# Performance work log

Hardware: AMD Instinct MI355X
Metric: run time of the kernel (lower is better)

## Reference

```python
import jax, jax.numpy as jnp
import numpy as np
import math

E = 2048         # n_embd
H = 16           # num query head pairs (num_heads)
HKV = 8          # num_kv_heads
NREP = H // HKV  # 2
HD = E // H // 2 # head_dim = 64
DEPTH = 12
LAMBDA_INIT = 0.8 - 0.6 * math.exp(-0.3 * DEPTH)
EPS = 1e-6


def setup_inputs() -> dict:
    key = jax.random.key(0)
    ks = jax.random.split(key, 10)
    s = lambda fan_in: 1.0 / np.sqrt(fan_in)
    return {
        "x": jax.random.normal(ks[0], (2, 2048, E), jnp.float32),
        "Wq": jax.random.normal(ks[1], (E, E), jnp.float32) * s(E),
        "Wk": jax.random.normal(ks[2], (E, E // NREP), jnp.float32) * s(E),
        "Wv": jax.random.normal(ks[3], (E, E // NREP), jnp.float32) * s(E),
        "Wo": jax.random.normal(ks[4], (E, E), jnp.float32) * s(E),
        "lam_q1": jax.random.normal(ks[5], (HD,), jnp.float32) * 0.1,
        "lam_k1": jax.random.normal(ks[6], (HD,), jnp.float32) * 0.1,
        "lam_q2": jax.random.normal(ks[7], (HD,), jnp.float32) * 0.1,
        "lam_k2": jax.random.normal(ks[8], (HD,), jnp.float32) * 0.1,
        "g": jnp.ones((2 * HD,), jnp.float32),  # RMSNorm weight
    }


def _rotary(x, cos, sin):
    # x: [B, T, nh, HD]; cos/sin: [T, HD//2]
    d = x.shape[-1] // 2
    x1, x2 = x[..., :d], x[..., d:]
    c = cos[None, :, None, :]
    si = sin[None, :, None, :]
    return jnp.concatenate([x1 * c + x2 * si, -x1 * si + x2 * c], axis=-1)


def reference(x, Wq, Wk, Wv, Wo, lam_q1, lam_k1, lam_q2, lam_k2, g):
    B, T, _ = x.shape
    q = (x @ Wq).reshape(B, T, 2 * H, HD)
    k = (x @ Wk).reshape(B, T, 2 * HKV, HD)
    v = (x @ Wv).reshape(B, T, HKV, 2 * HD)

    inv_freq = 1.0 / (10000.0 ** (jnp.arange(0, HD, 2, dtype=jnp.float32) / HD))
    freqs = jnp.arange(T, dtype=jnp.float32)[:, None] * inv_freq[None, :]
    cos, sin = jnp.cos(freqs), jnp.sin(freqs)
    q = _rotary(q, cos, sin)
    k = _rotary(k, cos, sin)

    q = jnp.transpose(q, (0, 2, 1, 3)) * (HD ** -0.5)   # [B, 2H, T, HD]
    k = jnp.repeat(jnp.transpose(k, (0, 2, 1, 3)), NREP, axis=1)  # [B, 2H, T, HD]
    v = jnp.repeat(jnp.transpose(v, (0, 2, 1, 3)), NREP, axis=1)  # [B, H, T, 2HD]

    scores = jnp.einsum('bhtd,bhsd->bhts', q, k)
    scores = jnp.nan_to_num(scores)
    mask = jnp.triu(jnp.full((T, T), -jnp.inf, scores.dtype), 1)
    scores = scores + mask
    p = jax.nn.softmax(scores.astype(jnp.float32), axis=-1).astype(scores.dtype)

    lam1 = jnp.exp(jnp.sum(lam_q1 * lam_k1))
    lam2 = jnp.exp(jnp.sum(lam_q2 * lam_k2))
    lam = lam1 - lam2 + LAMBDA_INIT

    p = p.reshape(B, H, 2, T, T)
    diff = p[:, :, 0] - lam * p[:, :, 1]               # [B, H, T, T]
    attn = jnp.einsum('bhts,bhsd->bhtd', diff, v)      # [B, H, T, 2HD]

    # RMSNorm over last dim (2*HD)
    attn = attn * jax.lax.rsqrt(jnp.mean(attn * attn, axis=-1, keepdims=True) + EPS) * g
    attn = attn * (1.0 - LAMBDA_INIT)
    attn = jnp.transpose(attn, (0, 2, 1, 3)).reshape(B, T, E)
    return attn @ Wo
```

## Files before the change

### kernel.cpp

```cpp
#include <hip/hip_runtime.h>

#define T_SEQ 2048

typedef __bf16 bf16x8 __attribute__((ext_vector_type(8)));
typedef float f32x4 __attribute__((ext_vector_type(4)));
typedef unsigned short u16;

__device__ __forceinline__ u16 f2b(float f) {
  unsigned u = __float_as_uint(f);
  unsigned r = 0x7fffu + ((u >> 16) & 1u);
  return (u16)((u + r) >> 16);
}
__device__ __forceinline__ float b2f(u16 v) {
  return __uint_as_float(((unsigned)v) << 16);
}
__device__ __forceinline__ f32x4 mfma16(bf16x8 a, bf16x8 b, f32x4 c) {
  return __builtin_amdgcn_mfma_f32_16x16x32_bf16(a, b, c, 0, 0, 0);
}
__device__ __forceinline__ void glds16(const void* g, void* s) {
  __builtin_amdgcn_global_load_lds(
      (const __attribute__((address_space(1))) void*)(uintptr_t)g,
      (__attribute__((address_space(3))) void*)(unsigned)(uintptr_t)s, 16, 0, 0);
}

__global__ void lam_kernel(const float* __restrict__ q1, const float* __restrict__ k1,
                           const float* __restrict__ q2, const float* __restrict__ k2,
                           float* __restrict__ outp) {
  int l = threadIdx.x;
  float a = q1[l] * k1[l];
  float c = q2[l] * k2[l];
  #pragma unroll
  for (int off = 32; off > 0; off >>= 1) {
    a += __shfl_down(a, off);
    c += __shfl_down(c, off);
  }
  if (l == 0) outp[0] = expf(a) - expf(c) + 0.7836057665316244f;
}

__global__ __launch_bounds__(256) void convert_kernel(const float* __restrict__ in,
                                                      u16* __restrict__ outp, int n) {
  int i = (blockIdx.x * 256 + threadIdx.x) * 4;
  if (i >= n) return;
  float4 v = *(const float4*)(in + i);
  ushort4 pk;
  pk.x = f2b(v.x); pk.y = f2b(v.y); pk.z = f2b(v.z); pk.w = f2b(v.w);
  *(ushort4*)(outp + i) = pk;
}

__global__ __launch_bounds__(256) void transpose_kernel(const float* __restrict__ in,
                                                        u16* __restrict__ outp, int R, int C) {
  __shared__ float tile[32][33];
  int c0 = blockIdx.x * 32, r0 = blockIdx.y * 32;
  int tx = threadIdx.x & 31, ty = threadIdx.x >> 5;
  #pragma unroll
  for (int k2 = 0; k2 < 4; k2++)
    tile[ty * 4 + k2][tx] = in[(size_t)(r0 + ty * 4 + k2) * C + c0 + tx];
  __syncthreads();
  #pragma unroll
  for (int k2 = 0; k2 < 4; k2++)
    outp[(size_t)(c0 + ty * 4 + k2) * R + r0 + tx] = f2b(tile[tx][ty * 4 + k2]);
}

template <bool OUT_BF16>
__global__ __launch_bounds__(256) void gemm128_kernel(const u16* __restrict__ A,
                                                      const u16* __restrict__ BT,
                                                      void* __restrict__ C, int N, int K) {
  __shared__ alignas(16) u16 As[128 * 64];
  __shared__ alignas(16) u16 Bs[128 * 64];
  const int tid = threadIdx.x, w = tid >> 6, lane = tid & 63;
  const int l15 = lane & 15, quad = lane >> 4;
  const int m0 = blockIdx.y * 128, n0 = blockIdx.x * 128;
  const int wm = (w >> 1) * 64, wn = (w & 1) * 64;
  const int lr = lane >> 3, slot = lane & 7, csw = slot ^ lr;
  f32x4 acc[4][4];
  #pragma unroll
  for (int mt = 0; mt < 4; mt++)
    #pragma unroll
    for (int nt = 0; nt < 4; nt++) acc[mt][nt] = (f32x4){0.f, 0.f, 0.f, 0.f};
  const u16* Ag = A + (size_t)(m0 + w * 32 + lr) * K + csw * 8;
  const u16* Bg = BT + (size_t)(n0 + w * 32 + lr) * K + csw * 8;
  u16* Asd = As + (w * 32) * 64;
  u16* Bsd = Bs + (w * 32) * 64;
  for (int kt = 0; kt < K; kt += 64) {
    #pragma unroll
    for (int i = 0; i < 4; i++) {
      glds16(Ag + kt + (size_t)(i * 8) * K, Asd + i * 512);
      glds16(Bg + kt + (size_t)(i * 8) * K, Bsd + i * 512);
    }
    __syncthreads();
    #pragma unroll
    for (int kk = 0; kk < 2; kk++) {
      bf16x8 am[4], bn[4];
      #pragma unroll
      for (int t = 0; t < 4; t++) {
        const int ra = wm + t * 16 + l15;
        am[t] = *(const bf16x8*)&As[ra * 64 + (((kk * 4 + quad) ^ (ra & 7)) << 3)];
        const int rb = wn + t * 16 + l15;
        bn[t] = *(const bf16x8*)&Bs[rb * 64 + (((kk * 4 + quad) ^ (rb & 7)) << 3)];
      }
      #pragma unroll
      for (int mt = 0; mt < 4; mt++)
        #pragma unroll
        for (int nt = 0; nt < 4; nt++) acc[mt][nt] = mfma16(am[mt], bn[nt], acc[mt][nt]);
    }
    __syncthreads();
  }
  const int row = m0 + wm + quad * 4;
  #pragma unroll
  for (int mt = 0; mt < 4; mt++) {
    #pragma unroll
    for (int nt = 0; nt < 4; nt++) {
      const int col = n0 + wn + nt * 16 + l15;
      #pragma unroll
      for (int rr = 0; rr < 4; rr++) {
        if (OUT_BF16)
          ((u16*)C)[(size_t)(row + mt * 16 + rr) * N + col] = f2b(acc[mt][nt][rr]);
        else
          ((float*)C)[(size_t)(row + mt * 16 + rr) * N + col] = acc[mt][nt][rr];
      }
    }
  }
}

__global__ __launch_bounds__(256) void rotary_kernel(const u16* __restrict__ qkv,
                                                     u16* __restrict__ outp, int lh,
                                                     int colbase, float scale) {
  int idx = blockIdx.x * 256 + threadIdx.x;
  int i = idx & 31;
  int h = (idx >> 5) & ((1 << lh) - 1);
  int bt = idx >> (5 + lh);
  int t = bt & (T_SEQ - 1);
  size_t inb = (size_t)bt * 4096 + colbase + h * 64 + i;
  float x1 = b2f(qkv[inb]);
  float x2 = b2f(qkv[inb + 32]);
  float invf = exp2f(-(float)i * 0.4152410118609203f);
  float ang = (float)t * invf;
  float c = cosf(ang), s = sinf(ang);
  float o1 = (x1 * c + x2 * s) * scale;
  float o2 = (x2 * c - x1 * s) * scale;
  size_t ob = ((size_t)((bt >> 11) * (1 << lh) + h) * T_SEQ + t) * 64 + i;
  outp[ob] = f2b(o1);
  outp[ob + 32] = f2b(o2);
}

__global__ __launch_bounds__(256) void vtrans_kernel(const u16* __restrict__ qkv,
                                                     u16* __restrict__ outp) {
  __shared__ unsigned tile[32][33];
  int bh = blockIdx.z;
  int t0 = blockIdx.x * 32, dv0 = blockIdx.y * 32;
  int tx = threadIdx.x & 31, ty = threadIdx.x >> 5;
  int bt_base = (bh >> 3) * T_SEQ;
  int col = 3072 + (bh & 7) * 128 + dv0 + tx;
  #pragma unroll
  for (int k2 = 0; k2 < 4; k2++)
    tile[ty * 4 + k2][tx] = qkv[(size_t)(bt_base + t0 + ty * 4 + k2) * 4096 + col];
  __syncthreads();
  #pragma unroll
  for (int k2 = 0; k2 < 4; k2++)
    outp[((size_t)bh * 128 + dv0 + ty * 4 + k2) * T_SEQ + t0 + tx] = (u16)tile[tx][ty * 4 + k2];
}

__global__ __launch_bounds__(256) void attn_kernel(const u16* __restrict__ Qb,
                                                   const u16* __restrict__ Kb,
                                                   const u16* __restrict__ Vt,
                                                   const float* __restrict__ lamp,
                                                   const float* __restrict__ g,
                                                   u16* __restrict__ attn_out) {
  __shared__ alignas(16) u16 Ks[64 * 64];
  __shared__ alignas(16) u16 Vs[128 * 64];
  __shared__ alignas(16) u16 Ps[4][16][72];
  const int pr = blockIdx.x;
  const int bh = blockIdx.y;
  const int b = bh >> 4, h = bh & 15;
  const int tid = threadIdx.x, w = tid >> 6, lane = tid & 63;
  const int l15 = lane & 15, quad = lane >> 4;
  const int lr = lane >> 3, slot = lane & 7, csw = slot ^ lr;
  const float lam = lamp[0];

  const u16* Kbase = Kb + (size_t)(b * 16 + h) * T_SEQ * 64;
  const u16* Vbase = Vt + (size_t)(b * 8 + (h >> 1)) * 128 * T_SEQ;
  const u16* Kg = Kbase + (size_t)(w * 16 + lr) * 64 + csw * 8;
  const u16* Vg = Vbase + (size_t)(w * 32 + lr) * T_SEQ + csw * 8;

  #pragma unroll 1
  for (int half = 0; half < 2; half++) {
    const int tt = half ? 31 - pr : pr;
    const int qb = tt * 64 + w * 16;

    bf16x8 qf[2][2];
    #pragma unroll
    for (int e = 0; e < 2; e++)
      #pragma unroll
      for (int kk = 0; kk < 2; kk++)
        qf[e][kk] = *(const bf16x8*)&Qb[((size_t)(b * 32 + 2 * h + e) * T_SEQ + qb + l15) * 64 +
                                        kk * 32 + quad * 8];

    f32x4 o[2][8];
    float lst[2][4];
    #pragma unroll
    for (int e = 0; e < 2; e++) {
      #pragma unroll
      for (int nt = 0; nt < 8; nt++) o[e][nt] = (f32x4){0.f, 0.f, 0.f, 0.f};
      #pragma unroll
      for (int rr = 0; rr < 4; rr++) lst[e][rr] = 0.f;
    }

    for (int st = 0; st <= tt; st++) {
      const int s0 = st * 64;
      glds16(Kg + (size_t)s0 * 64, &Ks[(w * 16) * 64]);
      glds16(Kg + (size_t)(s0 + 8) * 64, &Ks[(w * 16 + 8) * 64]);
      #pragma unroll
      for (int i = 0; i < 4; i++)
        glds16(Vg + s0 + (size_t)(i * 8) * T_SEQ, &Vs[(w * 32 + i * 8) * 64]);
      __syncthreads();

      bf16x8 kf[4][2];
      #pragma unroll
      for (int j = 0; j < 4; j++) {
        const int rk = j * 16 + l15;
        #pragma unroll
        for (int kk = 0; kk < 2; kk++)
          kf[j][kk] = *(const bf16x8*)&Ks[rk * 64 + (((kk * 4 + quad) ^ (rk & 7)) << 3)];
      }

      bf16x8 pa[2][2];
      #pragma unroll
      for (int e = 0; e < 2; e++) {
        f32x4 sc[4];
        #pragma unroll
        for (int j = 0; j < 4; j++) {
          f32x4 z = {0.f, 0.f, 0.f, 0.f};
          z = mfma16(qf[e][0], kf[j][0], z);
          sc[j] = mfma16(qf[e][1], kf[j][1], z);
        }
        if (st == tt) {
          #pragma unroll
          for (int j = 0; j < 4; j++) {
            int scol = s0 + j * 16 + l15;
            #pragma unroll
            for (int rr = 0; rr < 4; rr++)
              if (scol > qb + quad * 4 + rr) sc[j][rr] = -1e30f;
          }
        }
        #pragma unroll
        for (int j = 0; j < 4; j++)
          #pragma unroll
          for (int rr = 0; rr < 4; rr++) {
            float p = __expf(sc[j][rr]);
            sc[j][rr] = p;
            lst[e][rr] += p;
          }
        asm volatile("" ::: "memory");
        #pragma unroll
        for (int j = 0; j < 4; j++)
          #pragma unroll
          for (int rr = 0; rr < 4; rr++)
            Ps[w][quad * 4 + rr][j * 16 + l15] = f2b(sc[j][rr]);
        asm volatile("s_waitcnt lgkmcnt(0)" ::: "memory");
        pa[e][0] = *(const bf16x8*)&Ps[w][l15][quad * 8];
        pa[e][1] = *(const bf16x8*)&Ps[w][l15][32 + quad * 8];
        asm volatile("" ::: "memory");
      }
      #pragma unroll
      for (int nt = 0; nt < 8; nt++) {
        const int rv = nt * 16 + l15;
        bf16x8 vf0 = *(const bf16x8*)&Vs[rv * 64 + ((quad ^ (rv & 7)) << 3)];
        bf16x8 vf1 = *(const bf16x8*)&Vs[rv * 64 + (((4 + quad) ^ (rv & 7)) << 3)];
        o[0][nt] = mfma16(pa[0][0], vf0, o[0][nt]);
        o[0][nt] = mfma16(pa[0][1], vf1, o[0][nt]);
        o[1][nt] = mfma16(pa[1][0], vf0, o[1][nt]);
        o[1][nt] = mfma16(pa[1][1], vf1, o[1][nt]);
      }
      __syncthreads();
    }

    #pragma unroll
    for (int e = 0; e < 2; e++)
      #pragma unroll
      for (int rr = 0; rr < 4; rr++) {
        float v = lst[e][rr];
        #pragma unroll
        for (int off = 1; off <= 8; off <<= 1) v += __shfl_xor(v, off);
        lst[e][rr] = v;
      }
    float il0[4], il1[4];
    #pragma unroll
    for (int rr = 0; rr < 4; rr++) {
      il0[rr] = 1.f / lst[0][rr];
      il1[rr] = lam / lst[1][rr];
    }
    float ssq[4] = {0.f, 0.f, 0.f, 0.f};
    #pragma unroll
    for (int nt = 0; nt < 8; nt++)
      #pragma unroll
      for (int rr = 0; rr < 4; rr++) {
        float v = o[0][nt][rr] * il0[rr] - o[1][nt][rr] * il1[rr];
        o[0][nt][rr] = v;
        ssq[rr] += v * v;
      }
    #pragma unroll
    for (int rr = 0; rr < 4; rr++) {
      #pragma unroll
      for (int off = 1; off <= 8; off <<= 1) ssq[rr] += __shfl_xor(ssq[rr], off);
    }
    float rsc[4];
    #pragma unroll
    for (int rr = 0; rr < 4; rr++)
      rsc[rr] = rsqrtf(ssq[rr] * (1.f / 128.f) + 1e-6f) * 0.2163942334683756f;
    #pragma unroll
    for (int nt = 0; nt < 8; nt++) {
      float gv = g[nt * 16 + l15];
      #pragma unroll
      for (int rr = 0; rr < 4; rr++) {
        float v = o[0][nt][rr] * rsc[rr] * gv;
        attn_out[(size_t)(b * T_SEQ + qb + quad * 4 + rr) * 2048 + h * 128 + nt * 16 + l15] =
            f2b(v);
      }
    }
    __syncthreads();
  }
}

extern "C" void kernel_launch(void* const* d_in, const int* in_sizes, int n_in, void* d_out,
                              int out_size, void* d_ws, size_t ws_size, hipStream_t stream) {
  const float* x = (const float*)d_in[0];
  const float* Wq = (const float*)d_in[1];
  const float* Wk = (const float*)d_in[2];
  const float* Wv = (const float*)d_in[3];
  const float* Wo = (const float*)d_in[4];
  const float* lq1 = (const float*)d_in[5];
  const float* lk1 = (const float*)d_in[6];
  const float* lq2 = (const float*)d_in[7];
  const float* lk2 = (const float*)d_in[8];
  const float* g = (const float*)d_in[9];

  char* ws = (char*)d_ws;
  u16* WT = (u16*)(ws);
  u16* WoT = (u16*)(ws + 16777216);
  u16* xbf = (u16*)(ws + 25165824);
  u16* QKV = (u16*)(ws + 41943040);
  u16* Qb = (u16*)(ws + 75497472);
  u16* Kb = (u16*)(ws + 92274688);
  u16* Vt = (u16*)(ws + 100663296);
  u16* Attn = (u16*)(ws + 109051904);
  float* lam = (float*)(ws + 125829120);

  lam_kernel<<<1, 64, 0, stream>>>(lq1, lk1, lq2, lk2, lam);
  convert_kernel<<<8192, 256, 0, stream>>>(x, xbf, 8388608);
  transpose_kernel<<<dim3(64, 64), 256, 0, stream>>>(Wq, WT, 2048, 2048);
  transpose_kernel<<<dim3(32, 64), 256, 0, stream>>>(Wk, WT + (size_t)2048 * 2048, 2048, 1024);
  transpose_kernel<<<dim3(32, 64), 256, 0, stream>>>(Wv, WT + (size_t)3072 * 2048, 2048, 1024);
  transpose_kernel<<<dim3(64, 64), 256, 0, stream>>>(Wo, WoT, 2048, 2048);
  gemm128_kernel<true><<<dim3(32, 32), 256, 0, stream>>>(xbf, WT, QKV, 4096, 2048);
  rotary_kernel<<<16384, 256, 0, stream>>>(QKV, Qb, 5, 0, 0.125f);
  rotary_kernel<<<8192, 256, 0, stream>>>(QKV, Kb, 4, 2048, 1.0f);
  vtrans_kernel<<<dim3(64, 4, 16), 256, 0, stream>>>(QKV, Vt);
  attn_kernel<<<dim3(16, 32), 256, 0, stream>>>(Qb, Kb, Vt, lam, g, Attn);
  gemm128_kernel<false><<<dim3(16, 32), 256, 0, stream>>>(Attn, WoT, d_out, 2048, 2048);
}
```

Measured before the change: 385.1 us.

## Transpose attention MFMA operands so scores map per-lane and pack P writes

Swaps the MFMA operand order in both the QK and PV products, so each lane holds one query row. Row sums then accumulate per lane, and P is written to LDS as packed 64-bit truncated-bf16 stores, with both heads' tiles staged together. The log2e factor is folded into the Q scale so exp2f replaces __expf. Output now goes through LDS and is written as 16-byte coalesced stores. The change targets ALU, shuffle and scattered-store overhead in the softmax and epilogue, at the cost of a larger P buffer and truncation instead of rounding for P.

```diff
diff --git a/kernel.cpp b/kernel.cpp
--- a/kernel.cpp
+++ b/kernel.cpp
@@ -16,6 +16,9 @@
 }
 __device__ __forceinline__ f32x4 mfma16(bf16x8 a, bf16x8 b, f32x4 c) {
   return __builtin_amdgcn_mfma_f32_16x16x32_bf16(a, b, c, 0, 0, 0);
+}
+__device__ __forceinline__ unsigned pkhi(float lo, float hi) {
+  return __builtin_amdgcn_perm(__float_as_uint(hi), __float_as_uint(lo), 0x07060302u);
 }
 __device__ __forceinline__ void glds16(const void* g, void* s) {
   __builtin_amdgcn_global_load_lds(
@@ -168,7 +171,7 @@
                                                    u16* __restrict__ attn_out) {
   __shared__ alignas(16) u16 Ks[64 * 64];
   __shared__ alignas(16) u16 Vs[128 * 64];
-  __shared__ alignas(16) u16 Ps[4][16][72];
+  __shared__ alignas(16) u16 Ps[4][16][136];
   const int pr = blockIdx.x;
   const int bh = blockIdx.y;
   const int b = bh >> 4, h = bh & 15;
@@ -186,6 +189,7 @@
   for (int half = 0; half < 2; half++) {
     const int tt = half ? 31 - pr : pr;
     const int qb = tt * 64 + w * 16;
+    const int qglob = qb + l15;
 
     bf16x8 qf[2][2];
     #pragma unroll
@@ -196,14 +200,11 @@
                                         kk * 32 + quad * 8];
 
     f32x4 o[2][8];
-    float lst[2][4];
-    #pragma unroll
-    for (int e = 0; e < 2; e++) {
+    float lsum[2] = {0.f, 0.f};
+    #pragma unroll
+    for (int e = 0; e < 2; e++)
       #pragma unroll
       for (int nt = 0; nt < 8; nt++) o[e][nt] = (f32x4){0.f, 0.f, 0.f, 0.f};
-      #pragma unroll
-      for (int rr = 0; rr < 4; rr++) lst[e][rr] = 0.f;
-    }
 
     for (int st = 0; st <= tt; st++) {
       const int s0 = st * 64;
@@ -223,99 +224,93 @@
           kf[j][kk] = *(const bf16x8*)&Ks[rk * 64 + (((kk * 4 + quad) ^ (rk & 7)) << 3)];
       }
 
-      bf16x8 pa[2][2];
       #pragma unroll
       for (int e = 0; e < 2; e++) {
         f32x4 sc[4];
         #pragma unroll
         for (int j = 0; j < 4; j++) {
           f32x4 z = {0.f, 0.f, 0.f, 0.f};
-          z = mfma16(qf[e][0], kf[j][0], z);
-          sc[j] = mfma16(qf[e][1], kf[j][1], z);
+          z = mfma16(kf[j][0], qf[e][0], z);
+          sc[j] = mfma16(kf[j][1], qf[e][1], z);
         }
         if (st == tt) {
           #pragma unroll
           for (int j = 0; j < 4; j++) {
-            int scol = s0 + j * 16 + l15;
+            int srow = s0 + j * 16 + quad * 4;
             #pragma unroll
             for (int rr = 0; rr < 4; rr++)
-              if (scol > qb + quad * 4 + rr) sc[j][rr] = -1e30f;
+              if (srow + rr > qglob) sc[j][rr] = -1e30f;
           }
         }
-        #pragma unroll
-        for (int j = 0; j < 4; j++)
+        float ls = 0.f;
+        #pragma unroll
+        for (int j = 0; j < 4; j++) {
           #pragma unroll
           for (int rr = 0; rr < 4; rr++) {
-            float p = __expf(sc[j][rr]);
+            float p = exp2f(sc[j][rr]);
             sc[j][rr] = p;
-            lst[e][rr] += p;
+            ls += p;
           }
-        asm volatile("" ::: "memory");
-        #pragma unroll
-        for (int j = 0; j < 4; j++)
-          #pragma unroll
-          for (int rr = 0; rr < 4; rr++)
-            Ps[w][quad * 4 + rr][j * 16 + l15] = f2b(sc[j][rr]);
-        asm volatile("s_waitcnt lgkmcnt(0)" ::: "memory");
-        pa[e][0] = *(const bf16x8*)&Ps[w][l15][quad * 8];
-        pa[e][1] = *(const bf16x8*)&Ps[w][l15][32 + quad * 8];
-        asm volatile("" ::: "memory");
-      }
+          uint2 pk;
+          pk.x = pkhi(sc[j][0], sc[j][1]);
+          pk.y = pkhi(sc[j][2], sc[j][3]);
+          *(uint2*)&Ps[w][l15][e * 64 + j * 16 + quad * 4] = pk;
+        }
+        lsum[e] += ls;
+      }
+      asm volatile("s_waitcnt lgkmcnt(0)" ::: "memory");
+      bf16x8 pa[2][2];
+      #pragma unroll
+      for (int e = 0; e < 2; e++)
+        #pragma unroll
+        for (int kk = 0; kk < 2; kk++)
+          pa[e][kk] = *(const bf16x8*)&Ps[w][l15][e * 64 + kk * 32 + quad * 8];
+      asm volatile("" ::: "memory");
       #pragma unroll
       for (int nt = 0; nt < 8; nt++) {
         const int rv = nt * 16 + l15;
         bf16x8 vf0 = *(const bf16x8*)&Vs[rv * 64 + ((quad ^ (rv & 7)) << 3)];
         bf16x8 vf1 = *(const bf16x8*)&Vs[rv * 64 + (((4 + quad) ^ (rv & 7)) << 3)];
-        o[0][nt] = mfma16(pa[0][0], vf0, o[0][nt]);
-        o[0][nt] = mfma16(pa[0][1], vf1, o[0][nt]);
-        o[1][nt] = mfma16(pa[1][0], vf0, o[1][nt]);
-        o[1][nt] = mfma16(pa[1][1], vf1, o[1][nt]);
+        o[0][nt] = mfma16(vf0, pa[0][0], o[0][nt]);
+        o[0][nt] = mfma16(vf1, pa[0][1], o[0][nt]);
+        o[1][nt] = mfma16(vf0, pa[1][0], o[1][nt]);
+        o[1][nt] = mfma16(vf1, pa[1][1], o[1][nt]);
       }
       __syncthreads();
     }
 
-    #pragma unroll
-    for (int e = 0; e < 2; e++)
+    float l0 = lsum[0], l1 = lsum[1];
+    l0 += __shfl_xor(l0, 16); l0 += __shfl_xor(l0, 32);
+    l1 += __shfl_xor(l1, 16); l1 += __shfl_xor(l1, 32);
+    const float il0 = 1.f / l0, il1 = lam / l1;
+    float ssq = 0.f;
+    #pragma unroll
+    for (int nt = 0; nt < 8; nt++)
       #pragma unroll
       for (int rr = 0; rr < 4; rr++) {
-        float v = lst[e][rr];
-        #pragma unroll
-        for (int off = 1; off <= 8; off <<= 1) v += __shfl_xor(v, off);
-        lst[e][rr] = v;
-      }
-    float il0[4], il1[4];
-    #pragma unroll
-    for (int rr = 0; rr < 4; rr++) {
-      il0[rr] = 1.f / lst[0][rr];
-      il1[rr] = lam / lst[1][rr];
-    }
-    float ssq[4] = {0.f, 0.f, 0.f, 0.f};
-    #pragma unroll
-    for (int nt = 0; nt < 8; nt++)
-      #pragma unroll
-      for (int rr = 0; rr < 4; rr++) {
-        float v = o[0][nt][rr] * il0[rr] - o[1][nt][rr] * il1[rr];
+        float v = o[0][nt][rr] * il0 - o[1][nt][rr] * il1;
         o[0][nt][rr] = v;
-        ssq[rr] += v * v;
-      }
-    #pragma unroll
-    for (int rr = 0; rr < 4; rr++) {
-      #pragma unroll
-      for (int off = 1; off <= 8; off <<= 1) ssq[rr] += __shfl_xor(ssq[rr], off);
-    }
-    float rsc[4];
-    #pragma unroll
-    for (int rr = 0; rr < 4; rr++)
-      rsc[rr] = rsqrtf(ssq[rr] * (1.f / 128.f) + 1e-6f) * 0.2163942334683756f;
+        ssq += v * v;
+      }
+    ssq += __shfl_xor(ssq, 16);
+    ssq += __shfl_xor(ssq, 32);
+    const float rsc = rsqrtf(ssq * (1.f / 128.f) + 1e-6f) * 0.2163942334683756f;
     #pragma unroll
     for (int nt = 0; nt < 8; nt++) {
-      float gv = g[nt * 16 + l15];
-      #pragma unroll
-      for (int rr = 0; rr < 4; rr++) {
-        float v = o[0][nt][rr] * rsc[rr] * gv;
-        attn_out[(size_t)(b * T_SEQ + qb + quad * 4 + rr) * 2048 + h * 128 + nt * 16 + l15] =
-            f2b(v);
-      }
+      float4 gv = *(const float4*)&g[nt * 16 + quad * 4];
+      uint2 pk;
+      pk.x = (unsigned)f2b(o[0][nt][0] * rsc * gv.x) |
+             ((unsigned)f2b(o[0][nt][1] * rsc * gv.y) << 16);
+      pk.y = (unsigned)f2b(o[0][nt][2] * rsc * gv.z) |
+             ((unsigned)f2b(o[0][nt][3] * rsc * gv.w) << 16);
+      *(uint2*)&Ps[w][l15][nt * 16 + quad * 4] = pk;
+    }
+    asm volatile("s_waitcnt lgkmcnt(0)" ::: "memory");
+    #pragma unroll
+    for (int i = 0; i < 4; i++) {
+      const int r = (lane >> 4) + i * 4, c = (lane & 15) * 8;
+      bf16x8 ov = *(const bf16x8*)&Ps[w][r][c];
+      *(bf16x8*)&attn_out[(size_t)(b * T_SEQ + qb + r) * 2048 + h * 128 + c] = ov;
     }
     __syncthreads();
   }
@@ -352,7 +347,7 @@
   transpose_kernel<<<dim3(32, 64), 256, 0, stream>>>(Wv, WT + (size_t)3072 * 2048, 2048, 1024);
   transpose_kernel<<<dim3(64, 64), 256, 0, stream>>>(Wo, WoT, 2048, 2048);
   gemm128_kernel<true><<<dim3(32, 32), 256, 0, stream>>>(xbf, WT, QKV, 4096, 2048);
-  rotary_kernel<<<16384, 256, 0, stream>>>(QKV, Qb, 5, 0, 0.125f);
+  rotary_kernel<<<16384, 256, 0, stream>>>(QKV, Qb, 5, 0, 0.18033688011112042f);
   rotary_kernel<<<8192, 256, 0, stream>>>(QKV, Kb, 4, 2048, 1.0f);
   vtrans_kernel<<<dim3(64, 4, 16), 256, 0, stream>>>(QKV, Vt);
   attn_kernel<<<dim3(16, 32), 256, 0, stream>>>(Qb, Kb, Vt, lam, g, Attn);
```

New measurement: 386.0 us. About the same (+0.2%).
